# Performance work log

Hardware: AMD Instinct MI355X
Metric: run time of the kernel (lower is better)

The kernel has to match this reference:

```python
import jax, jax.numpy as jnp
import numpy as np

N = 5000  # num_nodes = feature dim = num classes
E = 160000


def _gcn_conv(x, src, dst, W, b, n):
    # PyG GCNConv: h = D^{-1/2} (A + I) D^{-1/2} (x W) + b
    h = x @ W  # [n, out]
    loops = jnp.arange(n, dtype=src.dtype)
    s = jnp.concatenate([src, loops])
    d = jnp.concatenate([dst, loops])
    deg = jax.ops.segment_sum(jnp.ones_like(s, dtype=h.dtype), d, num_segments=n)
    inv_sqrt = jnp.where(deg > 0, jax.lax.rsqrt(deg), 0.0)
    coef = inv_sqrt[s] * inv_sqrt[d]  # [E+n]
    msgs = h[s] * coef[:, None]       # gather-scale
    out = jax.ops.segment_sum(msgs, d, num_segments=n)  # scatter-add
    return out + b


def setup_inputs() -> dict:
    key = jax.random.key(0)
    k1, k2, k3, k4, k5 = jax.random.split(key, 5)
    x = jax.random.normal(k1, (N, N), dtype=jnp.float32)
    src = jax.random.randint(k2, (E,), 0, N, dtype=jnp.int32)
    dst = jax.random.randint(k3, (E,), 0, N, dtype=jnp.int32)
    W1 = jax.random.normal(k4, (N, 16), dtype=jnp.float32) * (1.0 / np.sqrt(N))
    b1 = jnp.zeros((16,), dtype=jnp.float32)
    W2 = jax.random.normal(k5, (16, N), dtype=jnp.float32) * (1.0 / np.sqrt(16))
    b2 = jnp.zeros((N,), dtype=jnp.float32)
    return {"x": x, "src": src, "dst": dst, "W1": W1, "b1": b1, "W2": W2, "b2": b2}


def reference(x, src, dst, W1, b1, W2, b2):
    h = _gcn_conv(x, src, dst, W1, b1, N)
    h = jax.nn.relu(h)
    h = _gcn_conv(h, src, dst, W2, b2, N)
    return jax.nn.log_softmax(h, axis=1)
```

## Files before the change

### kernel.cpp

```cpp
#include <hip/hip_runtime.h>
#include <math.h>

#define NN 5000
#define NE 160000
#define NF 16
#define KS 640
#define WTS 648
#define CAP 128

typedef __attribute__((ext_vector_type(8))) short bf16x8;
typedef __attribute__((ext_vector_type(4))) float f32x4;


__device__ __forceinline__ short f2bf(float f) {
  union { float f; unsigned u; } v; v.f = f;
  unsigned r = v.u + 0x7FFFu + ((v.u >> 16) & 1u);
  return (short)(r >> 16);
}

__global__ void k_scatter(const int* __restrict__ src, const int* __restrict__ dst,
                          int* __restrict__ cur, int* __restrict__ slots) {
  int e = blockIdx.x * 256 + threadIdx.x;
  if (e >= NE) return;
  int d = dst[e];
  int pos = atomicAdd(&cur[d], 1);
  if (pos < CAP) slots[d * CAP + pos] = src[e];
}

__global__ __launch_bounds__(256) void k_gemm1(const float* __restrict__ x,
                                               const float* __restrict__ w1,
                                               float* __restrict__ h1) {
  __shared__ short wt[NF * WTS];
  const int tid = threadIdx.x;
  const int lane = tid & 63;
  const int wv = tid >> 6;
  const int kb = blockIdx.y * KS;
  const int klen = (NN - kb < KS) ? (NN - kb) : KS;
  const int nsteps = (klen + 31) >> 5;

  for (int kk = tid; kk < KS; kk += 256) {
    const int kg = kb + kk;
    if (kg < NN) {
      const float4* __restrict__ wr = (const float4*)(w1 + (size_t)kg * NF);
      const float4 a = wr[0], b = wr[1], c = wr[2], d = wr[3];
      wt[0 * WTS + kk] = f2bf(a.x);  wt[1 * WTS + kk] = f2bf(a.y);
      wt[2 * WTS + kk] = f2bf(a.z);  wt[3 * WTS + kk] = f2bf(a.w);
      wt[4 * WTS + kk] = f2bf(b.x);  wt[5 * WTS + kk] = f2bf(b.y);
      wt[6 * WTS + kk] = f2bf(b.z);  wt[7 * WTS + kk] = f2bf(b.w);
      wt[8 * WTS + kk] = f2bf(c.x);  wt[9 * WTS + kk] = f2bf(c.y);
      wt[10 * WTS + kk] = f2bf(c.z); wt[11 * WTS + kk] = f2bf(c.w);
      wt[12 * WTS + kk] = f2bf(d.x); wt[13 * WTS + kk] = f2bf(d.y);
      wt[14 * WTS + kk] = f2bf(d.z); wt[15 * WTS + kk] = f2bf(d.w);
    } else {
#pragma unroll
      for (int n = 0; n < NF; ++n) wt[n * WTS + kk] = 0;
    }
  }
  __syncthreads();

  const int tile = blockIdx.x * 4 + wv;
  const int m0 = tile * 16;
  int arow = m0 + (lane & 15);
  if (arow > NN - 1) arow = NN - 1;
  const float* __restrict__ xr = x + (size_t)arow * NN + kb;
  const int quad = lane >> 4;
  const short* __restrict__ bp = &wt[(lane & 15) * WTS + quad * 8];

  f32x4 acc = {0.f, 0.f, 0.f, 0.f};
  for (int s = 0; s < nsteps; ++s) {
    const int k0 = s * 32 + quad * 8;
    bf16x8 a;
    if (kb + k0 < NN) {
      const float4 xa = *(const float4*)(xr + k0);
      const float4 xb = *(const float4*)(xr + k0 + 4);
      a[0] = f2bf(xa.x); a[1] = f2bf(xa.y); a[2] = f2bf(xa.z); a[3] = f2bf(xa.w);
      a[4] = f2bf(xb.x); a[5] = f2bf(xb.y); a[6] = f2bf(xb.z); a[7] = f2bf(xb.w);
    } else {
#pragma unroll
      for (int j = 0; j < 8; ++j) a[j] = 0;
    }
    const bf16x8 b = *(const bf16x8*)(bp + s * 32);
    acc = __builtin_amdgcn_mfma_f32_16x16x32_bf16(a, b, acc, 0, 0, 0);
  }

  const int col = lane & 15;
#pragma unroll
  for (int r = 0; r < 4; ++r) {
    const int orow = m0 + quad * 4 + r;
    if (orow < NN) atomicAdd(&h1[orow * NF + col], acc[r]);
  }
}

template <int RELU>
__global__ __launch_bounds__(256) void k_gather(const int* __restrict__ slots,
                                                const int* __restrict__ cnt,
                                                const float* __restrict__ bias,
                                                const float* __restrict__ hin,
                                                float* __restrict__ outp) {
  const int tid = threadIdx.x;
  const int lane = tid & 63;
  const int wv = tid >> 6;
  const int v = blockIdx.x * 4 + wv;
  if (v >= NN) return;
  const int j = lane & 15;
  const int eg = lane >> 4;
  int deg = cnt[v];
  if (deg > CAP) deg = CAP;
  const int* __restrict__ sl = slots + v * CAP;

  float acc = 0.f;
  int base = 0;
  for (; base + 8 <= deg; base += 8) {
    const int s0 = sl[base + eg];
    const int s1 = sl[base + 4 + eg];
    const float iv0 = rsqrtf((float)cnt[s0] + 1.0f);
    const float iv1 = rsqrtf((float)cnt[s1] + 1.0f);
    acc += iv0 * hin[s0 * NF + j];
    acc += iv1 * hin[s1 * NF + j];
  }
  for (; base < deg; base += 4) {
    const int idx = base + eg;
    if (idx < deg) {
      const int s = sl[idx];
      acc += rsqrtf((float)cnt[s] + 1.0f) * hin[s * NF + j];
    }
  }
  acc += __shfl_xor(acc, 16);
  acc += __shfl_xor(acc, 32);

  if (lane < 16) {
    const float ivv = rsqrtf((float)deg + 1.0f);
    float r = ivv * acc + ivv * ivv * hin[v * NF + j];
    if constexpr (RELU) r = fmaxf(r + bias[j], 0.f);
    outp[v * NF + j] = r;
  }
}

__global__ __launch_bounds__(512) void k_final(const float* __restrict__ g2,
                                               const float* __restrict__ w2,
                                               const float* __restrict__ b2,
                                               float* __restrict__ out) {
  __shared__ float zs[4 * NN];
  __shared__ float gsh[64];
  __shared__ float red[8 * 4];
  __shared__ float rowmax[4];
  __shared__ float rowoff[4];
  const int tid = threadIdx.x;
  const int lane = tid & 63;
  const int wv = tid >> 6;
  const int row0 = blockIdx.x * 4;

  if (tid < 64) gsh[tid] = g2[row0 * NF + tid];
  __syncthreads();
  float g[4][NF];
#pragma unroll
  for (int r = 0; r < 4; ++r)
#pragma unroll
    for (int k = 0; k < NF; ++k) g[r][k] = gsh[r * NF + k];

  float mx[4] = {-1e30f, -1e30f, -1e30f, -1e30f};
  for (int jc = tid; jc < NN; jc += 512) {
    float w[NF];
#pragma unroll
    for (int k = 0; k < NF; ++k) w[k] = w2[k * NN + jc];
    const float bb = b2[jc];
#pragma unroll
    for (int r = 0; r < 4; ++r) {
      float z = bb;
#pragma unroll
      for (int k = 0; k < NF; ++k) z = fmaf(g[r][k], w[k], z);
      zs[r * NN + jc] = z;
      mx[r] = fmaxf(mx[r], z);
    }
  }
#pragma unroll
  for (int r = 0; r < 4; ++r) {
    float m = mx[r];
    for (int off = 32; off; off >>= 1) m = fmaxf(m, __shfl_xor(m, off));
    if (lane == 0) red[wv * 4 + r] = m;
  }
  __syncthreads();
  if (tid < 4) {
    float m = red[tid];
#pragma unroll
    for (int w = 1; w < 8; ++w) m = fmaxf(m, red[w * 4 + tid]);
    rowmax[tid] = m;
  }
  __syncthreads();
  const float rm0 = rowmax[0], rm1 = rowmax[1], rm2 = rowmax[2], rm3 = rowmax[3];

  float sm[4] = {0.f, 0.f, 0.f, 0.f};
  for (int jc = tid; jc < NN; jc += 512) {
    sm[0] += __expf(zs[0 * NN + jc] - rm0);
    sm[1] += __expf(zs[1 * NN + jc] - rm1);
    sm[2] += __expf(zs[2 * NN + jc] - rm2);
    sm[3] += __expf(zs[3 * NN + jc] - rm3);
  }
#pragma unroll
  for (int r = 0; r < 4; ++r) {
    float s = sm[r];
    for (int off = 32; off; off >>= 1) s += __shfl_xor(s, off);
    if (lane == 0) red[wv * 4 + r] = s;
  }
  __syncthreads();
  if (tid < 4) {
    float s = red[tid];
#pragma unroll
    for (int w = 1; w < 8; ++w) s += red[w * 4 + tid];
    rowoff[tid] = rowmax[tid] + logf(s);
  }
  __syncthreads();
  const float o0 = rowoff[0], o1 = rowoff[1], o2 = rowoff[2], o3 = rowoff[3];
  for (int jc = tid; jc < NN; jc += 512) {
    out[(size_t)(row0 + 0) * NN + jc] = zs[0 * NN + jc] - o0;
    out[(size_t)(row0 + 1) * NN + jc] = zs[1 * NN + jc] - o1;
    out[(size_t)(row0 + 2) * NN + jc] = zs[2 * NN + jc] - o2;
    out[(size_t)(row0 + 3) * NN + jc] = zs[3 * NN + jc] - o3;
  }
}

extern "C" void kernel_launch(void* const* d_in, const int* in_sizes, int n_in,
                              void* d_out, int out_size, void* d_ws, size_t ws_size,
                              hipStream_t stream) {
  const float* x  = (const float*)d_in[0];
  const int*   src = (const int*)d_in[1];
  const int*   dst = (const int*)d_in[2];
  const float* W1 = (const float*)d_in[3];
  const float* b1 = (const float*)d_in[4];
  const float* W2 = (const float*)d_in[5];
  const float* b2 = (const float*)d_in[6];
  float* out = (float*)d_out;

  char* ws = (char*)d_ws;
  int*   cur   = (int*)(ws);
  float* h1    = (float*)(ws + 20000);
  int*   slots = (int*)(ws + 340000);
  float* a1    = (float*)(ws + 2900000);
  float* g2    = (float*)(ws + 3220000);

  hipMemsetAsync(d_ws, 0, 340000, stream);
  k_scatter<<<(NE + 255) / 256, 256, 0, stream>>>(src, dst, cur, slots);
  k_gemm1<<<dim3(79, 8), 256, 0, stream>>>(x, W1, h1);
  k_gather<1><<<NN / 4, 256, 0, stream>>>(slots, cur, b1, h1, a1);
  k_gather<0><<<NN / 4, 256, 0, stream>>>(slots, cur, nullptr, a1, g2);
  k_final<<<NN / 4, 512, 0, stream>>>(g2, W2, b2, out);
}
```

Baseline: 252.3 us.

## Fuse edge scatter into GEMM launch and second gather into final softmax kernel

The edge-bucketing scatter is folded into the first GEMM launch as extra blocks, and the second-layer neighbor aggregation is computed inside the final W2 + log-softmax kernel. That kernel now runs 1024 threads with one row per thread group. This cuts the launch count from five to three and drops the g2 round trip through global memory. The cost is a larger block that has to do a gather phase before the dense work, plus extra reductions across 16 waves.

```diff
diff --git a/kernel.cpp b/kernel.cpp
--- a/kernel.cpp
+++ b/kernel.cpp
@@ -7,6 +7,8 @@
 #define KS 640
 #define WTS 648
 #define CAP 128
+#define SCB 625
+#define GMB 632
 
 typedef __attribute__((ext_vector_type(8))) short bf16x8;
 typedef __attribute__((ext_vector_type(4))) float f32x4;
@@ -18,23 +20,33 @@
   return (short)(r >> 16);
 }
 
-__global__ void k_scatter(const int* __restrict__ src, const int* __restrict__ dst,
-                          int* __restrict__ cur, int* __restrict__ slots) {
-  int e = blockIdx.x * 256 + threadIdx.x;
-  if (e >= NE) return;
-  int d = dst[e];
-  int pos = atomicAdd(&cur[d], 1);
-  if (pos < CAP) slots[d * CAP + pos] = src[e];
-}
-
-__global__ __launch_bounds__(256) void k_gemm1(const float* __restrict__ x,
-                                               const float* __restrict__ w1,
-                                               float* __restrict__ h1) {
+__global__ __launch_bounds__(256) void k_gemm_scat(const float* __restrict__ x,
+                                                   const float* __restrict__ w1,
+                                                   float* __restrict__ h1,
+                                                   const int* __restrict__ src,
+                                                   const int* __restrict__ dst,
+                                                   int* __restrict__ cur,
+                                                   int* __restrict__ slots) {
   __shared__ short wt[NF * WTS];
+  const int bid = blockIdx.x;
   const int tid = threadIdx.x;
+
+  if (bid < SCB) {
+    const int e = bid * 256 + tid;
+    if (e < NE) {
+      const int d = dst[e];
+      const int pos = atomicAdd(&cur[d], 1);
+      if (pos < CAP) slots[d * CAP + pos] = src[e];
+    }
+    return;
+  }
+
+  const int gb = bid - SCB;
+  const int bx = gb % 79;
+  const int by = gb / 79;
   const int lane = tid & 63;
   const int wv = tid >> 6;
-  const int kb = blockIdx.y * KS;
+  const int kb = by * KS;
   const int klen = (NN - kb < KS) ? (NN - kb) : KS;
   const int nsteps = (klen + 31) >> 5;
 
@@ -58,7 +70,7 @@
   }
   __syncthreads();
 
-  const int tile = blockIdx.x * 4 + wv;
+  const int tile = bx * 4 + wv;
   const int m0 = tile * 16;
   int arow = m0 + (lane & 15);
   if (arow > NN - 1) arow = NN - 1;
@@ -91,12 +103,11 @@
   }
 }
 
-template <int RELU>
-__global__ __launch_bounds__(256) void k_gather(const int* __restrict__ slots,
-                                                const int* __restrict__ cnt,
-                                                const float* __restrict__ bias,
-                                                const float* __restrict__ hin,
-                                                float* __restrict__ outp) {
+__global__ __launch_bounds__(256) void k_gather1(const int* __restrict__ slots,
+                                                 const int* __restrict__ cnt,
+                                                 const float* __restrict__ bias,
+                                                 const float* __restrict__ hin,
+                                                 float* __restrict__ outp) {
   const int tid = threadIdx.x;
   const int lane = tid & 63;
   const int wv = tid >> 6;
@@ -131,18 +142,20 @@
   if (lane < 16) {
     const float ivv = rsqrtf((float)deg + 1.0f);
     float r = ivv * acc + ivv * ivv * hin[v * NF + j];
-    if constexpr (RELU) r = fmaxf(r + bias[j], 0.f);
-    outp[v * NF + j] = r;
-  }
-}
-
-__global__ __launch_bounds__(512) void k_final(const float* __restrict__ g2,
-                                               const float* __restrict__ w2,
-                                               const float* __restrict__ b2,
-                                               float* __restrict__ out) {
+    outp[v * NF + j] = fmaxf(r + bias[j], 0.f);
+  }
+}
+
+__global__ __launch_bounds__(1024) void k_final2(const int* __restrict__ slots,
+                                                 const int* __restrict__ cnt,
+                                                 const float* __restrict__ a1,
+                                                 const float* __restrict__ w2,
+                                                 const float* __restrict__ b2,
+                                                 float* __restrict__ out) {
   __shared__ float zs[4 * NN];
-  __shared__ float gsh[64];
-  __shared__ float red[8 * 4];
+  __shared__ float pp[16][NF];
+  __shared__ float gsh[4 * NF];
+  __shared__ float red[16 * 4];
   __shared__ float rowmax[4];
   __shared__ float rowoff[4];
   const int tid = threadIdx.x;
@@ -150,72 +163,85 @@
   const int wv = tid >> 6;
   const int row0 = blockIdx.x * 4;
 
-  if (tid < 64) gsh[tid] = g2[row0 * NF + tid];
-  __syncthreads();
-  float g[4][NF];
-#pragma unroll
-  for (int r = 0; r < 4; ++r)
-#pragma unroll
-    for (int k = 0; k < NF; ++k) g[r][k] = gsh[r * NF + k];
-
-  float mx[4] = {-1e30f, -1e30f, -1e30f, -1e30f};
-  for (int jc = tid; jc < NN; jc += 512) {
-    float w[NF];
-#pragma unroll
-    for (int k = 0; k < NF; ++k) w[k] = w2[k * NN + jc];
-    const float bb = b2[jc];
-#pragma unroll
-    for (int r = 0; r < 4; ++r) {
-      float z = bb;
-#pragma unroll
-      for (int k = 0; k < NF; ++k) z = fmaf(g[r][k], w[k], z);
+  {
+    const int r = wv >> 2;
+    const int v = row0 + r;
+    const int j = lane & 15;
+    const int sg = ((wv & 3) << 2) | (lane >> 4);
+    int deg = cnt[v];
+    if (deg > CAP) deg = CAP;
+    const int* __restrict__ sl = slots + v * CAP;
+    float acc = 0.f;
+    for (int idx = sg; idx < deg; idx += 16) {
+      const int s = sl[idx];
+      acc += rsqrtf((float)cnt[s] + 1.0f) * a1[s * NF + j];
+    }
+    acc += __shfl_xor(acc, 16);
+    acc += __shfl_xor(acc, 32);
+    if (lane < 16) pp[wv][j] = acc;
+  }
+  __syncthreads();
+  if (tid < 64) {
+    const int r = tid >> 4, j = tid & 15;
+    const int v = row0 + r;
+    int deg = cnt[v];
+    if (deg > CAP) deg = CAP;
+    const float ivv = rsqrtf((float)deg + 1.0f);
+    const float acc = pp[r * 4 + 0][j] + pp[r * 4 + 1][j] +
+                      pp[r * 4 + 2][j] + pp[r * 4 + 3][j];
+    gsh[r * NF + j] = ivv * acc + ivv * ivv * a1[v * NF + j];
+  }
+  __syncthreads();
+
+  const int r = tid & 3;
+  const int jb = tid >> 2;
+  float gr[NF];
+#pragma unroll
+  for (int k = 0; k < NF; ++k) gr[k] = gsh[r * NF + k];
+
+  float mx = -1e30f;
+  for (int c = 0, jc = jb; c < 20; ++c, jc += 256) {
+    if (jc < NN) {
+      float z = b2[jc];
+#pragma unroll
+      for (int k = 0; k < NF; ++k) z = fmaf(gr[k], w2[k * NN + jc], z);
       zs[r * NN + jc] = z;
-      mx[r] = fmaxf(mx[r], z);
-    }
-  }
-#pragma unroll
-  for (int r = 0; r < 4; ++r) {
-    float m = mx[r];
-    for (int off = 32; off; off >>= 1) m = fmaxf(m, __shfl_xor(m, off));
-    if (lane == 0) red[wv * 4 + r] = m;
-  }
+      mx = fmaxf(mx, z);
+    }
+  }
+#pragma unroll
+  for (int off = 32; off >= 4; off >>= 1) mx = fmaxf(mx, __shfl_xor(mx, off));
+  if (lane < 4) red[wv * 4 + lane] = mx;
   __syncthreads();
   if (tid < 4) {
     float m = red[tid];
 #pragma unroll
-    for (int w = 1; w < 8; ++w) m = fmaxf(m, red[w * 4 + tid]);
+    for (int w = 1; w < 16; ++w) m = fmaxf(m, red[w * 4 + tid]);
     rowmax[tid] = m;
   }
   __syncthreads();
-  const float rm0 = rowmax[0], rm1 = rowmax[1], rm2 = rowmax[2], rm3 = rowmax[3];
-
-  float sm[4] = {0.f, 0.f, 0.f, 0.f};
-  for (int jc = tid; jc < NN; jc += 512) {
-    sm[0] += __expf(zs[0 * NN + jc] - rm0);
-    sm[1] += __expf(zs[1 * NN + jc] - rm1);
-    sm[2] += __expf(zs[2 * NN + jc] - rm2);
-    sm[3] += __expf(zs[3 * NN + jc] - rm3);
-  }
-#pragma unroll
-  for (int r = 0; r < 4; ++r) {
-    float s = sm[r];
-    for (int off = 32; off; off >>= 1) s += __shfl_xor(s, off);
-    if (lane == 0) red[wv * 4 + r] = s;
-  }
+
+  const float rm = rowmax[r];
+  float sm = 0.f;
+  for (int c = 0, jc = jb; c < 20; ++c, jc += 256) {
+    if (jc < NN) sm += __expf(zs[r * NN + jc] - rm);
+  }
+#pragma unroll
+  for (int off = 32; off >= 4; off >>= 1) sm += __shfl_xor(sm, off);
+  if (lane < 4) red[wv * 4 + lane] = sm;
   __syncthreads();
   if (tid < 4) {
     float s = red[tid];
 #pragma unroll
-    for (int w = 1; w < 8; ++w) s += red[w * 4 + tid];
+    for (int w = 1; w < 16; ++w) s += red[w * 4 + tid];
     rowoff[tid] = rowmax[tid] + logf(s);
   }
   __syncthreads();
-  const float o0 = rowoff[0], o1 = rowoff[1], o2 = rowoff[2], o3 = rowoff[3];
-  for (int jc = tid; jc < NN; jc += 512) {
-    out[(size_t)(row0 + 0) * NN + jc] = zs[0 * NN + jc] - o0;
-    out[(size_t)(row0 + 1) * NN + jc] = zs[1 * NN + jc] - o1;
-    out[(size_t)(row0 + 2) * NN + jc] = zs[2 * NN + jc] - o2;
-    out[(size_t)(row0 + 3) * NN + jc] = zs[3 * NN + jc] - o3;
+
+  const float off_r = rowoff[r];
+  float* __restrict__ orow = out + (size_t)(row0 + r) * NN;
+  for (int c = 0, jc = jb; c < 20; ++c, jc += 256) {
+    if (jc < NN) orow[jc] = zs[r * NN + jc] - off_r;
   }
 }
 
@@ -236,12 +262,9 @@
   float* h1    = (float*)(ws + 20000);
   int*   slots = (int*)(ws + 340000);
   float* a1    = (float*)(ws + 2900000);
-  float* g2    = (float*)(ws + 3220000);
 
   hipMemsetAsync(d_ws, 0, 340000, stream);
-  k_scatter<<<(NE + 255) / 256, 256, 0, stream>>>(src, dst, cur, slots);
-  k_gemm1<<<dim3(79, 8), 256, 0, stream>>>(x, W1, h1);
-  k_gather<1><<<NN / 4, 256, 0, stream>>>(slots, cur, b1, h1, a1);
-  k_gather<0><<<NN / 4, 256, 0, stream>>>(slots, cur, nullptr, a1, g2);
-  k_final<<<NN / 4, 512, 0, stream>>>(g2, W2, b2, out);
-}
+  k_gemm_scat<<<SCB + GMB, 256, 0, stream>>>(x, W1, h1, src, dst, cur, slots);
+  k_gather1<<<NN / 4, 256, 0, stream>>>(slots, cur, b1, h1, a1);
+  k_final2<<<NN / 4, 1024, 0, stream>>>(slots, cur, a1, W2, b2, out);
+}
```

After: 274.4 us. 1.09x slower.
